# Kernel tuning notes

Hardware: AMD Instinct MI355X
Metric: run time of the kernel (lower is better)

The kernel has to match this reference:

```python
import jax, jax.numpy as jnp
import numpy as np

D = 1024
H = 16
FF = 4096
N, L = 16, 512
EPS = 1e-5


def _layernorm(x, g, b):
    mu = jnp.mean(x, axis=-1, keepdims=True)
    var = jnp.mean(jnp.square(x - mu), axis=-1, keepdims=True)
    return (x - mu) * jax.lax.rsqrt(var + EPS) * g + b


def setup_inputs() -> dict:
    key = jax.random.key(0)
    ks = jax.random.split(key, 8)
    std = 0.02  # truncated-normal-ish init scale
    return {
        "x": jax.random.normal(ks[0], (N, L, D), dtype=jnp.float32),
        "mask": jnp.zeros((N, L, L), dtype=bool),  # True = padded position
        "WQ": jax.random.normal(ks[1], (D, D), dtype=jnp.float32) * std,
        "bQ": jnp.zeros((D,), jnp.float32),
        "WK": jax.random.normal(ks[2], (D, D), dtype=jnp.float32) * std,
        "bK": jnp.zeros((D,), jnp.float32),
        "WV": jax.random.normal(ks[3], (D, D), dtype=jnp.float32) * std,
        "bV": jnp.zeros((D,), jnp.float32),
        "WO": jax.random.normal(ks[4], (D, D), dtype=jnp.float32) * std,
        "bO": jnp.zeros((D,), jnp.float32),
        "ln0_g": jnp.ones((D,), jnp.float32),
        "ln0_b": jnp.zeros((D,), jnp.float32),
        "W1": jax.random.normal(ks[5], (D, FF), dtype=jnp.float32) * std,
        "b1": jnp.zeros((FF,), jnp.float32),
        "W2": jax.random.normal(ks[6], (FF, D), dtype=jnp.float32) * std,
        "b2": jnp.zeros((D,), jnp.float32),
        "ln1_g": jnp.ones((D,), jnp.float32),
        "ln1_b": jnp.zeros((D,), jnp.float32),
    }


def reference(x, mask, WQ, bQ, WK, bK, WV, bV, WO, bO, ln0_g, ln0_b,
              W1, b1, W2, b2, ln1_g, ln1_b):
    n, l, d = x.shape
    dk = d // H
    scale = jnp.sqrt(jnp.float32(dk))
    # QKV projections -> [n, H, l, dk]
    q = (x @ WQ + bQ).reshape(n, l, H, dk).transpose(0, 2, 1, 3)
    k = (x @ WK + bK).reshape(n, l, H, dk).transpose(0, 2, 1, 3)
    v = (x @ WV + bV).reshape(n, l, H, dk).transpose(0, 2, 1, 3)
    scores = jnp.einsum('nhqd,nhkd->nhqk', q, k) / scale
    scores = jnp.where(mask[:, None, :, :], -jnp.inf, scores)
    attn = jax.nn.softmax(scores, axis=-1)
    attn = jnp.nan_to_num(attn, nan=0.0)  # fully-masked rows -> 0
    ctx = jnp.einsum('nhqk,nhkd->nhqd', attn, v).transpose(0, 2, 1, 3).reshape(n, l, d)
    mha = ctx @ WO + bO
    h = _layernorm(mha + x, ln0_g, ln0_b)
    ff = jax.nn.gelu(h @ W1 + b1, approximate=False) @ W2 + b2
    return _layernorm(ff + h, ln1_g, ln1_b)
```

## Files before the change

kernel.cpp:

```cpp
#include <hip/hip_runtime.h>
#include <math.h>

#define D_   1024
#define H_   16
#define DK_  64
#define L_   512
#define NB_  16
#define FF_  4096
#define M_   (NB_*L_)
#define EPS_ 1e-5f

typedef __attribute__((ext_vector_type(8))) __bf16 bf16x8;
typedef __attribute__((ext_vector_type(4))) float f32x4;
typedef __attribute__((ext_vector_type(4))) unsigned short us4;
typedef __attribute__((ext_vector_type(8))) unsigned short us8;
typedef __attribute__((ext_vector_type(4))) unsigned int u32x4;

__device__ __forceinline__ float gelu_exact(float x){
    return 0.5f * x * (1.f + erff(x * 0.7071067811865476f));
}

__device__ __forceinline__ unsigned split1(float a){
    unsigned ab = __builtin_bit_cast(unsigned, a);
    unsigned short h = (unsigned short)(ab >> 16);
    float hif = __builtin_bit_cast(float, ab & 0xffff0000u);
    float rem = a - hif;
    unsigned short lo = (unsigned short)(__builtin_bit_cast(unsigned, rem) >> 16);
    return (unsigned)h | ((unsigned)lo << 16);
}

__device__ __forceinline__ void split4v(float4 x, us4& h, us4& lo){
    unsigned p0 = split1(x.x), p1 = split1(x.y), p2 = split1(x.z), p3 = split1(x.w);
    h.x = (unsigned short)p0; lo.x = (unsigned short)(p0 >> 16);
    h.y = (unsigned short)p1; lo.y = (unsigned short)(p1 >> 16);
    h.z = (unsigned short)p2; lo.z = (unsigned short)(p2 >> 16);
    h.w = (unsigned short)p3; lo.w = (unsigned short)(p3 >> 16);
}

__device__ __forceinline__ void split8v(float4 x, float4 y, bf16x8& h, bf16x8& lo){
    us8 hu, lu; unsigned p;
    p = split1(x.x); hu[0]=(unsigned short)p; lu[0]=(unsigned short)(p>>16);
    p = split1(x.y); hu[1]=(unsigned short)p; lu[1]=(unsigned short)(p>>16);
    p = split1(x.z); hu[2]=(unsigned short)p; lu[2]=(unsigned short)(p>>16);
    p = split1(x.w); hu[3]=(unsigned short)p; lu[3]=(unsigned short)(p>>16);
    p = split1(y.x); hu[4]=(unsigned short)p; lu[4]=(unsigned short)(p>>16);
    p = split1(y.y); hu[5]=(unsigned short)p; lu[5]=(unsigned short)(p>>16);
    p = split1(y.z); hu[6]=(unsigned short)p; lu[6]=(unsigned short)(p>>16);
    p = split1(y.w); hu[7]=(unsigned short)p; lu[7]=(unsigned short)(p>>16);
    h = __builtin_bit_cast(bf16x8, hu);
    lo = __builtin_bit_cast(bf16x8, lu);
}

template<int EPI>
__global__ __launch_bounds__(256, 2)
void gemm_mfma(const float* __restrict__ A, const float* __restrict__ B,
               const float* __restrict__ bias, const float* __restrict__ res,
               float* __restrict__ C, int M, int N, int K)
{
    __shared__ __align__(16) unsigned short Ah[4096];
    __shared__ __align__(16) unsigned short Al[4096];
    __shared__ __align__(16) unsigned short Bh[4096];
    __shared__ __align__(16) unsigned short Bl[4096];

    const int t = threadIdx.x;
    const int bm = blockIdx.y * 128, bn = blockIdx.x * 128;
    const int l = t & 63, w = t >> 6, wr = w >> 1, wc = w & 1;

    size_t gA[4]; int lA[4];
#pragma unroll
    for (int i = 0; i < 4; ++i) {
        int f = t + 256 * i;
        int r = f >> 3, k0 = (f & 7) * 4;
        gA[i] = (size_t)(bm + r) * K + k0;
        lA[i] = ((r >> 4) << 9) + (((k0 >> 3) << 4) + (r & 15)) * 8 + (k0 & 7);
    }
    const int c = t & 127, kq = t >> 7;
    const size_t gB = (size_t)(kq * 16) * N + bn + c;
    const int lB = ((c >> 4) << 9) + (kq * 2 * 16 + (c & 15)) * 8;

    f32x4 acc[4][4] = {};

    float4 aA[4];
    float  bB[16];
#pragma unroll
    for (int i = 0; i < 4; ++i) aA[i] = *(const float4*)&A[gA[i]];
#pragma unroll
    for (int i = 0; i < 16; ++i) bB[i] = B[gB + (size_t)i * N];

    const int nk = K >> 5;
    for (int ks = 0; ks < nk; ++ks) {
        __syncthreads();
#pragma unroll
        for (int i = 0; i < 4; ++i) {
            us4 h, lo;
            split4v(aA[i], h, lo);
            *(us4*)&Ah[lA[i]] = h;
            *(us4*)&Al[lA[i]] = lo;
        }
        {
            us8 h0, l0, h1, l1;
#pragma unroll
            for (int i = 0; i < 8; ++i) {
                unsigned p = split1(bB[i]);
                h0[i] = (unsigned short)p; l0[i] = (unsigned short)(p >> 16);
            }
#pragma unroll
            for (int i = 0; i < 8; ++i) {
                unsigned p = split1(bB[8 + i]);
                h1[i] = (unsigned short)p; l1[i] = (unsigned short)(p >> 16);
            }
            *(us8*)&Bh[lB] = h0;       *(us8*)&Bl[lB] = l0;
            *(us8*)&Bh[lB + 128] = h1; *(us8*)&Bl[lB + 128] = l1;
        }
        __syncthreads();
        if (ks + 1 < nk) {
            const int ko = (ks + 1) * 32;
#pragma unroll
            for (int i = 0; i < 4; ++i) aA[i] = *(const float4*)&A[gA[i] + ko];
#pragma unroll
            for (int i = 0; i < 16; ++i) bB[i] = B[gB + (size_t)(ko + i) * N];
        }
        bf16x8 ah[4], al4[4];
#pragma unroll
        for (int m = 0; m < 4; ++m) {
            const int idx = (wr * 4 + m) * 512 + l * 8;
            ah[m]  = *(const bf16x8*)&Ah[idx];
            al4[m] = *(const bf16x8*)&Al[idx];
        }
#pragma unroll
        for (int n = 0; n < 4; ++n) {
            const int idx = (wc * 4 + n) * 512 + l * 8;
            bf16x8 bh = *(const bf16x8*)&Bh[idx];
            bf16x8 bl = *(const bf16x8*)&Bl[idx];
#pragma unroll
            for (int m = 0; m < 4; ++m) {
                acc[m][n] = __builtin_amdgcn_mfma_f32_16x16x32_bf16(ah[m],  bh, acc[m][n], 0, 0, 0);
                acc[m][n] = __builtin_amdgcn_mfma_f32_16x16x32_bf16(ah[m],  bl, acc[m][n], 0, 0, 0);
                acc[m][n] = __builtin_amdgcn_mfma_f32_16x16x32_bf16(al4[m], bh, acc[m][n], 0, 0, 0);
            }
        }
    }

#pragma unroll
    for (int n = 0; n < 4; ++n) {
        const int col = bn + wc * 64 + n * 16 + (l & 15);
        const float bv = bias[col];
#pragma unroll
        for (int m = 0; m < 4; ++m) {
            const int rowb = bm + wr * 64 + m * 16 + ((l >> 4) << 2);
#pragma unroll
            for (int j = 0; j < 4; ++j) {
                const int row = rowb + j;
                float v = acc[m][n][j] + bv;
                if (EPI == 0) {
                    const int nb = row >> 9, ll = row & (L_ - 1);
                    const int hh = col >> 6, d = col & (DK_ - 1);
                    C[(((size_t)nb * H_ + hh) * L_ + ll) * DK_ + d] = v;
                } else if (EPI == 1) {
                    v += res[(size_t)row * N + col];
                    C[(size_t)row * N + col] = v;
                } else if (EPI == 2) {
                    C[(size_t)row * N + col] = gelu_exact(v);
                } else {
                    const int nb = row >> 9, ll = row & (L_ - 1);
                    const int hh = col >> 6, d = col & (DK_ - 1);
                    C[(((size_t)nb * H_ + hh) * DK_ + d) * L_ + ll] = v;
                }
            }
        }
    }
}

__global__ __launch_bounds__(512, 1)
void attn_mfma(const float* __restrict__ qb, const float* __restrict__ kb,
               const float* __restrict__ vt, const unsigned char* __restrict__ mask,
               float* __restrict__ ctx)
{
    __shared__ unsigned Sp[64 * 512];
    __shared__ __align__(16) unsigned short KVh[4096];
    __shared__ __align__(16) unsigned short KVl[4096];

    const int t = threadIdx.x;
    const int l = t & 63, w = t >> 6;
    const int qsub = w & 3;
    const int ksub = w >> 2;
    const int qt = blockIdx.x;
    const int nh = blockIdx.y;
    const int n = nh >> 4, hh = nh & 15;
    const int q0 = qt * 64;

    const float* qbase = qb + (size_t)nh * L_ * DK_;
    const float* kbase = kb + (size_t)nh * L_ * DK_;
    const float* vbase = vt + (size_t)nh * DK_ * L_;

    bf16x8 qh[2], ql[2];
#pragma unroll
    for (int ks = 0; ks < 2; ++ks) {
        const size_t qa = (size_t)(q0 + qsub * 16 + (l & 15)) * DK_ + ks * 32 + (l >> 4) * 8;
        float4 a0 = *(const float4*)&qbase[qa];
        float4 a1 = *(const float4*)&qbase[qa + 4];
        split8v(a0, a1, qh[ks], ql[ks]);
    }

    float4 pf[2];
#pragma unroll
    for (int i = 0; i < 2; ++i) {
        int f = t + 512 * i, r = f >> 4, k0 = (f & 15) * 4;
        pf[i] = *(const float4*)&kbase[(size_t)r * DK_ + k0];
    }
    for (int kt = 0; kt < 8; ++kt) {
        __syncthreads();
#pragma unroll
        for (int i = 0; i < 2; ++i) {
            int f = t + 512 * i, r = f >> 4, k0 = (f & 15) * 4;
            int off = (((r >> 4) * 2 + (k0 >> 5)) << 9) + ((((k0 & 31) >> 3) << 4) + (r & 15)) * 8 + (k0 & 7);
            us4 h, lo; split4v(pf[i], h, lo);
            *(us4*)&KVh[off] = h; *(us4*)&KVl[off] = lo;
        }
        __syncthreads();
        if (kt < 7) {
#pragma unroll
            for (int i = 0; i < 2; ++i) {
                int f = t + 512 * i, r = f >> 4, k0 = (f & 15) * 4;
                pf[i] = *(const float4*)&kbase[(size_t)((kt + 1) * 64 + r) * DK_ + k0];
            }
        }
        f32x4 acc2[2] = {};
#pragma unroll
        for (int ks = 0; ks < 2; ++ks) {
#pragma unroll
            for (int b = 0; b < 2; ++b) {
                const int off = (((ksub * 2 + b) * 2 + ks) << 9) + l * 8;
                bf16x8 bh = *(const bf16x8*)&KVh[off];
                bf16x8 bl = *(const bf16x8*)&KVl[off];
                acc2[b] = __builtin_amdgcn_mfma_f32_16x16x32_bf16(qh[ks], bh, acc2[b], 0, 0, 0);
                acc2[b] = __builtin_amdgcn_mfma_f32_16x16x32_bf16(qh[ks], bl, acc2[b], 0, 0, 0);
                acc2[b] = __builtin_amdgcn_mfma_f32_16x16x32_bf16(ql[ks], bh, acc2[b], 0, 0, 0);
            }
        }
#pragma unroll
        for (int b = 0; b < 2; ++b) {
            const int col = kt * 64 + (ksub * 2 + b) * 16 + (l & 15);
#pragma unroll
            for (int j = 0; j < 4; ++j) {
                const int row = qsub * 16 + (l >> 4) * 4 + j;
                const int word = row * 512 + ((((col >> 2) ^ (row & 7)) << 2) | (col & 3));
                Sp[word] = split1(acc2[b][j] * 0.125f);
            }
        }
    }
    __syncthreads();

    {
        const int row = t >> 3, seg = t & 7;
        const unsigned* mrow = (const unsigned*)(mask + ((size_t)n * L_ + q0 + row) * L_ + seg * 64);
        unsigned mb[16];
#pragma unroll
        for (int j2 = 0; j2 < 16; ++j2) mb[j2] = mrow[j2];
        float sum = 0.f;
#pragma unroll
        for (int i = 0; i < 64; ++i) {
            const int col = seg * 64 + i;
            const int word = row * 512 + ((((col >> 2) ^ (row & 7)) << 2) | (i & 3));
            unsigned u = Sp[word];
            float val = __builtin_bit_cast(float, (u & 0xffffu) << 16)
                      + __builtin_bit_cast(float, u & 0xffff0000u);
            if (!((mb[i >> 2] >> ((i & 3) * 8)) & 0xffu)) sum += __expf(val);
        }
        sum += __shfl_xor(sum, 1); sum += __shfl_xor(sum, 2); sum += __shfl_xor(sum, 4);
        const float inv = sum > 0.f ? 1.f / sum : 0.f;
#pragma unroll
        for (int i = 0; i < 64; ++i) {
            const int col = seg * 64 + i;
            const int word = row * 512 + ((((col >> 2) ^ (row & 7)) << 2) | (i & 3));
            unsigned u = Sp[word];
            float val = __builtin_bit_cast(float, (u & 0xffffu) << 16)
                      + __builtin_bit_cast(float, u & 0xffff0000u);
            float p = ((mb[i >> 2] >> ((i & 3) * 8)) & 0xffu) ? 0.f : __expf(val) * inv;
            Sp[word] = split1(p);
        }
    }

    f32x4 oacc[2] = {};
#pragma unroll
    for (int i = 0; i < 2; ++i) {
        int f = t + 512 * i, d = f >> 4, key0 = (f & 15) * 4;
        pf[i] = *(const float4*)&vbase[(size_t)d * L_ + key0];
    }
    for (int kt = 0; kt < 8; ++kt) {
        __syncthreads();
#pragma unroll
        for (int i = 0; i < 2; ++i) {
            int f = t + 512 * i, d = f >> 4, key0 = (f & 15) * 4;
            int off = (((d >> 4) * 2 + (key0 >> 5)) << 9) + ((((key0 & 31) >> 3) << 4) + (d & 15)) * 8 + (key0 & 7);
            us4 h, lo; split4v(pf[i], h, lo);
            *(us4*)&KVh[off] = h; *(us4*)&KVl[off] = lo;
        }
        __syncthreads();
        if (kt < 7) {
#pragma unroll
            for (int i = 0; i < 2; ++i) {
                int f = t + 512 * i, d = f >> 4, key0 = (f & 15) * 4;
                pf[i] = *(const float4*)&vbase[(size_t)d * L_ + (kt + 1) * 64 + key0];
            }
        }
#pragma unroll
        for (int ks = 0; ks < 2; ++ks) {
            const int rowpv = qsub * 16 + (l & 15);
            const int sw = rowpv & 7;
            const int g0 = kt * 16 + ks * 8 + (l >> 4) * 2;
            u32x4 Ua = *(const u32x4*)&Sp[rowpv * 512 + ((g0 ^ sw) << 2)];
            u32x4 Ub = *(const u32x4*)&Sp[rowpv * 512 + (((g0 + 1) ^ sw) << 2)];
            us8 hu, lu;
            hu[0]=(unsigned short)Ua[0]; lu[0]=(unsigned short)(Ua[0]>>16);
            hu[1]=(unsigned short)Ua[1]; lu[1]=(unsigned short)(Ua[1]>>16);
            hu[2]=(unsigned short)Ua[2]; lu[2]=(unsigned short)(Ua[2]>>16);
            hu[3]=(unsigned short)Ua[3]; lu[3]=(unsigned short)(Ua[3]>>16);
            hu[4]=(unsigned short)Ub[0]; lu[4]=(unsigned short)(Ub[0]>>16);
            hu[5]=(unsigned short)Ub[1]; lu[5]=(unsigned short)(Ub[1]>>16);
            hu[6]=(unsigned short)Ub[2]; lu[6]=(unsigned short)(Ub[2]>>16);
            hu[7]=(unsigned short)Ub[3]; lu[7]=(unsigned short)(Ub[3]>>16);
            bf16x8 ph = __builtin_bit_cast(bf16x8, hu);
            bf16x8 pl = __builtin_bit_cast(bf16x8, lu);
#pragma unroll
            for (int b = 0; b < 2; ++b) {
                const int off = (((ksub * 2 + b) * 2 + ks) << 9) + l * 8;
                bf16x8 vh = *(const bf16x8*)&KVh[off];
                bf16x8 vl = *(const bf16x8*)&KVl[off];
                oacc[b] = __builtin_amdgcn_mfma_f32_16x16x32_bf16(ph, vh, oacc[b], 0, 0, 0);
                oacc[b] = __builtin_amdgcn_mfma_f32_16x16x32_bf16(ph, vl, oacc[b], 0, 0, 0);
                oacc[b] = __builtin_amdgcn_mfma_f32_16x16x32_bf16(pl, vh, oacc[b], 0, 0, 0);
            }
        }
    }
#pragma unroll
    for (int b = 0; b < 2; ++b) {
        const int col = ksub * 32 + b * 16 + (l & 15);
#pragma unroll
        for (int j = 0; j < 4; ++j) {
            const int rowl = q0 + qsub * 16 + (l >> 4) * 4 + j;
            ctx[((size_t)n * L_ + rowl) * D_ + hh * 64 + col] = oacc[b][j];
        }
    }
}

__global__ __launch_bounds__(256)
void ln_k(const float* __restrict__ in, const float* __restrict__ g,
          const float* __restrict__ b, float* __restrict__ out)
{
    const int row = blockIdx.x, tid = threadIdx.x;
    const float* p = in + (size_t)row * D_;
    float4 v = *(const float4*)&p[tid * 4];
    float s = v.x + v.y + v.z + v.w;
#pragma unroll
    for (int off = 32; off > 0; off >>= 1) s += __shfl_down(s, off);
    __shared__ float wsum[4];
    const int wid = tid >> 6, lane = tid & 63;
    if (lane == 0) wsum[wid] = s;
    __syncthreads();
    const float mu = (wsum[0] + wsum[1] + wsum[2] + wsum[3]) * (1.f / D_);
    const float dx = v.x - mu, dy = v.y - mu, dz = v.z - mu, dw = v.w - mu;
    float q = dx * dx + dy * dy + dz * dz + dw * dw;
#pragma unroll
    for (int off = 32; off > 0; off >>= 1) q += __shfl_down(q, off);
    __syncthreads();
    if (lane == 0) wsum[wid] = q;
    __syncthreads();
    const float var = (wsum[0] + wsum[1] + wsum[2] + wsum[3]) * (1.f / D_);
    const float rs = rsqrtf(var + EPS_);
    const float4 gg = *(const float4*)&g[tid * 4];
    const float4 bb = *(const float4*)&b[tid * 4];
    float4 o;
    o.x = dx * rs * gg.x + bb.x;
    o.y = dy * rs * gg.y + bb.y;
    o.z = dz * rs * gg.z + bb.z;
    o.w = dw * rs * gg.w + bb.w;
    *(float4*)&out[(size_t)row * D_ + tid * 4] = o;
}

extern "C" void kernel_launch(void* const* d_in, const int* in_sizes, int n_in,
                              void* d_out, int out_size, void* d_ws, size_t ws_size,
                              hipStream_t stream)
{
    const float* x  = (const float*)d_in[0];
    const unsigned char* mask = (const unsigned char*)d_in[1];
    const float* WQ = (const float*)d_in[2];
    const float* bQ = (const float*)d_in[3];
    const float* WK = (const float*)d_in[4];
    const float* bK = (const float*)d_in[5];
    const float* WV = (const float*)d_in[6];
    const float* bV = (const float*)d_in[7];
    const float* WO = (const float*)d_in[8];
    const float* bO = (const float*)d_in[9];
    const float* g0 = (const float*)d_in[10];
    const float* b0 = (const float*)d_in[11];
    const float* W1 = (const float*)d_in[12];
    const float* b1 = (const float*)d_in[13];
    const float* W2 = (const float*)d_in[14];
    const float* b2 = (const float*)d_in[15];
    const float* g1 = (const float*)d_in[16];
    const float* b1n = (const float*)d_in[17];
    float* out = (float*)d_out;

    const size_t MD = (size_t)M_ * D_;
    float* ws   = (float*)d_ws;
    float* qbuf = ws;
    float* kbuf = ws + MD;
    float* vbuf = ws + 2 * MD;
    float* cbuf = ws + 3 * MD;
    float* fbuf = ws + 4 * MD;
    float* hbuf = out;

    dim3 blk(256);
    dim3 gD(D_ / 128, M_ / 128);
    dim3 gF(FF_ / 128, M_ / 128);

    gemm_mfma<0><<<gD, blk, 0, stream>>>(x, WQ, bQ, nullptr, qbuf, M_, D_, D_);
    gemm_mfma<0><<<gD, blk, 0, stream>>>(x, WK, bK, nullptr, kbuf, M_, D_, D_);
    gemm_mfma<3><<<gD, blk, 0, stream>>>(x, WV, bV, nullptr, vbuf, M_, D_, D_);
    attn_mfma<<<dim3(L_ / 64, NB_ * H_), dim3(512), 0, stream>>>(qbuf, kbuf, vbuf, mask, cbuf);
    gemm_mfma<1><<<gD, blk, 0, stream>>>(cbuf, WO, bO, x, qbuf, M_, D_, D_);
    ln_k<<<dim3(M_), blk, 0, stream>>>(qbuf, g0, b0, hbuf);
    gemm_mfma<2><<<gF, blk, 0, stream>>>(hbuf, W1, b1, nullptr, fbuf, M_, FF_, D_);
    gemm_mfma<1><<<gD, blk, 0, stream>>>(fbuf, W2, b2, hbuf, kbuf, M_, D_, FF_);
    ln_k<<<dim3(M_), blk, 0, stream>>>(kbuf, g1, b1n, out);
}
```

Measured before the change: 1.109 ms.

## Pre-split weights into bf16 hi/lo tiles and stream them via global_load_lds

```diff
diff --git a/kernel.cpp b/kernel.cpp
--- a/kernel.cpp
+++ b/kernel.cpp
@@ -51,20 +51,51 @@
     lo = __builtin_bit_cast(bf16x8, lu);
 }
 
+__device__ __forceinline__ void gl16(const unsigned short* g, unsigned short* l){
+    __builtin_amdgcn_global_load_lds(
+        (const __attribute__((address_space(1))) unsigned int*)g,
+        (__attribute__((address_space(3))) unsigned int*)l, 16, 0, 0);
+}
+
+__global__ __launch_bounds__(256)
+void wsplit_k(const float* __restrict__ W, unsigned short* __restrict__ out,
+              int K, int N)
+{
+    const int ks = blockIdx.x, nb = blockIdx.y;
+    unsigned short* tb = out + ((size_t)nb * (K >> 5) + ks) * 8192;
+    const int t = threadIdx.x;
+#pragma unroll
+    for (int it = 0; it < 2; ++it) {
+        const int slot = t + it * 256;
+        const int c = slot & 127, ko = slot >> 7;
+        us8 h, lo;
+#pragma unroll
+        for (int j = 0; j < 8; ++j) {
+            float wv = W[(size_t)(ks * 32 + ko * 8 + j) * N + nb * 128 + c];
+            unsigned p = split1(wv);
+            h[j] = (unsigned short)p; lo[j] = (unsigned short)(p >> 16);
+        }
+        const int off = ((c >> 4) * 512) + (ko * 16 + (c & 15)) * 8;
+        *(us8*)&tb[off] = h;
+        *(us8*)&tb[4096 + off] = lo;
+    }
+}
+
 template<int EPI>
-__global__ __launch_bounds__(256, 2)
-void gemm_mfma(const float* __restrict__ A, const float* __restrict__ B,
+__global__ __launch_bounds__(256, 4)
+void gemm_mfma(const float* __restrict__ A, const unsigned short* __restrict__ Bw,
                const float* __restrict__ bias, const float* __restrict__ res,
                float* __restrict__ C, int M, int N, int K)
 {
-    __shared__ __align__(16) unsigned short Ah[4096];
-    __shared__ __align__(16) unsigned short Al[4096];
-    __shared__ __align__(16) unsigned short Bh[4096];
-    __shared__ __align__(16) unsigned short Bl[4096];
+    __shared__ __align__(16) unsigned short Ah[4160];
+    __shared__ __align__(16) unsigned short Al[4160];
+    __shared__ __align__(16) unsigned short Bs[8192];
 
     const int t = threadIdx.x;
-    const int bm = blockIdx.y * 128, bn = blockIdx.x * 128;
+    const int nb = blockIdx.x;
+    const int bm = blockIdx.y * 128, bn = nb * 128;
     const int l = t & 63, w = t >> 6, wr = w >> 1, wc = w & 1;
+    const int nk = K >> 5;
 
     size_t gA[4]; int lA[4];
 #pragma unroll
@@ -72,24 +103,23 @@
         int f = t + 256 * i;
         int r = f >> 3, k0 = (f & 7) * 4;
         gA[i] = (size_t)(bm + r) * K + k0;
-        lA[i] = ((r >> 4) << 9) + (((k0 >> 3) << 4) + (r & 15)) * 8 + (k0 & 7);
-    }
-    const int c = t & 127, kq = t >> 7;
-    const size_t gB = (size_t)(kq * 16) * N + bn + c;
-    const int lB = ((c >> 4) << 9) + (kq * 2 * 16 + (c & 15)) * 8;
+        lA[i] = (r >> 4) * 520 + (((k0 >> 3) << 4) + (r & 15)) * 8 + (k0 & 7);
+    }
+    const unsigned short* wtile = Bw + (size_t)nb * nk * 8192;
 
     f32x4 acc[4][4] = {};
 
     float4 aA[4];
-    float  bB[16];
 #pragma unroll
     for (int i = 0; i < 4; ++i) aA[i] = *(const float4*)&A[gA[i]];
-#pragma unroll
-    for (int i = 0; i < 16; ++i) bB[i] = B[gB + (size_t)i * N];
-
-    const int nk = K >> 5;
+
     for (int ks = 0; ks < nk; ++ks) {
         __syncthreads();
+        const unsigned short* tb = wtile + (size_t)ks * 8192;
+        gl16(tb + t * 8,        Bs + t * 8);
+        gl16(tb + 2048 + t * 8, Bs + 2048 + t * 8);
+        gl16(tb + 4096 + t * 8, Bs + 4096 + t * 8);
+        gl16(tb + 6144 + t * 8, Bs + 6144 + t * 8);
 #pragma unroll
         for (int i = 0; i < 4; ++i) {
             us4 h, lo;
@@ -97,41 +127,24 @@
             *(us4*)&Ah[lA[i]] = h;
             *(us4*)&Al[lA[i]] = lo;
         }
-        {
-            us8 h0, l0, h1, l1;
-#pragma unroll
-            for (int i = 0; i < 8; ++i) {
-                unsigned p = split1(bB[i]);
-                h0[i] = (unsigned short)p; l0[i] = (unsigned short)(p >> 16);
-            }
-#pragma unroll
-            for (int i = 0; i < 8; ++i) {
-                unsigned p = split1(bB[8 + i]);
-                h1[i] = (unsigned short)p; l1[i] = (unsigned short)(p >> 16);
-            }
-            *(us8*)&Bh[lB] = h0;       *(us8*)&Bl[lB] = l0;
-            *(us8*)&Bh[lB + 128] = h1; *(us8*)&Bl[lB + 128] = l1;
-        }
         __syncthreads();
         if (ks + 1 < nk) {
             const int ko = (ks + 1) * 32;
 #pragma unroll
             for (int i = 0; i < 4; ++i) aA[i] = *(const float4*)&A[gA[i] + ko];
-#pragma unroll
-            for (int i = 0; i < 16; ++i) bB[i] = B[gB + (size_t)(ko + i) * N];
         }
         bf16x8 ah[4], al4[4];
 #pragma unroll
         for (int m = 0; m < 4; ++m) {
-            const int idx = (wr * 4 + m) * 512 + l * 8;
+            const int idx = (wr * 4 + m) * 520 + l * 8;
             ah[m]  = *(const bf16x8*)&Ah[idx];
             al4[m] = *(const bf16x8*)&Al[idx];
         }
 #pragma unroll
         for (int n = 0; n < 4; ++n) {
             const int idx = (wc * 4 + n) * 512 + l * 8;
-            bf16x8 bh = *(const bf16x8*)&Bh[idx];
-            bf16x8 bl = *(const bf16x8*)&Bl[idx];
+            bf16x8 bh = *(const bf16x8*)&Bs[idx];
+            bf16x8 bl = *(const bf16x8*)&Bs[4096 + idx];
 #pragma unroll
             for (int m = 0; m < 4; ++m) {
                 acc[m][n] = __builtin_amdgcn_mfma_f32_16x16x32_bf16(ah[m],  bh, acc[m][n], 0, 0, 0);
@@ -153,18 +166,18 @@
                 const int row = rowb + j;
                 float v = acc[m][n][j] + bv;
                 if (EPI == 0) {
-                    const int nb = row >> 9, ll = row & (L_ - 1);
+                    const int nbx = row >> 9, ll = row & (L_ - 1);
                     const int hh = col >> 6, d = col & (DK_ - 1);
-                    C[(((size_t)nb * H_ + hh) * L_ + ll) * DK_ + d] = v;
+                    C[(((size_t)nbx * H_ + hh) * L_ + ll) * DK_ + d] = v;
                 } else if (EPI == 1) {
                     v += res[(size_t)row * N + col];
                     C[(size_t)row * N + col] = v;
                 } else if (EPI == 2) {
                     C[(size_t)row * N + col] = gelu_exact(v);
                 } else {
-                    const int nb = row >> 9, ll = row & (L_ - 1);
+                    const int nbx = row >> 9, ll = row & (L_ - 1);
                     const int hh = col >> 6, d = col & (DK_ - 1);
-                    C[(((size_t)nb * H_ + hh) * DK_ + d) * L_ + ll] = v;
+                    C[(((size_t)nbx * H_ + hh) * DK_ + d) * L_ + ll] = v;
                 }
             }
         }
@@ -411,17 +424,33 @@
     float* fbuf = ws + 4 * MD;
     float* hbuf = out;
 
+    unsigned short* WQs = (unsigned short*)fbuf;
+    unsigned short* WKs = WQs + 2ull * D_ * D_;
+    unsigned short* WVs = WQs + 4ull * D_ * D_;
+    unsigned short* WOs = WQs + 6ull * D_ * D_;
+    unsigned short* W1s = (unsigned short*)vbuf;
+    unsigned short* W2s = (unsigned short*)vbuf + 2ull * D_ * FF_;
+
     dim3 blk(256);
     dim3 gD(D_ / 128, M_ / 128);
     dim3 gF(FF_ / 128, M_ / 128);
 
-    gemm_mfma<0><<<gD, blk, 0, stream>>>(x, WQ, bQ, nullptr, qbuf, M_, D_, D_);
-    gemm_mfma<0><<<gD, blk, 0, stream>>>(x, WK, bK, nullptr, kbuf, M_, D_, D_);
-    gemm_mfma<3><<<gD, blk, 0, stream>>>(x, WV, bV, nullptr, vbuf, M_, D_, D_);
+    wsplit_k<<<dim3(D_ / 32, D_ / 128), blk, 0, stream>>>(WQ, WQs, D_, D_);
+    wsplit_k<<<dim3(D_ / 32, D_ / 128), blk, 0, stream>>>(WK, WKs, D_, D_);
+    wsplit_k<<<dim3(D_ / 32, D_ / 128), blk, 0, stream>>>(WV, WVs, D_, D_);
+    wsplit_k<<<dim3(D_ / 32, D_ / 128), blk, 0, stream>>>(WO, WOs, D_, D_);
+
+    gemm_mfma<0><<<gD, blk, 0, stream>>>(x, WQs, bQ, nullptr, qbuf, M_, D_, D_);
+    gemm_mfma<0><<<gD, blk, 0, stream>>>(x, WKs, bK, nullptr, kbuf, M_, D_, D_);
+    gemm_mfma<3><<<gD, blk, 0, stream>>>(x, WVs, bV, nullptr, vbuf, M_, D_, D_);
     attn_mfma<<<dim3(L_ / 64, NB_ * H_), dim3(512), 0, stream>>>(qbuf, kbuf, vbuf, mask, cbuf);
-    gemm_mfma<1><<<gD, blk, 0, stream>>>(cbuf, WO, bO, x, qbuf, M_, D_, D_);
+    gemm_mfma<1><<<gD, blk, 0, stream>>>(cbuf, WOs, bO, x, qbuf, M_, D_, D_);
     ln_k<<<dim3(M_), blk, 0, stream>>>(qbuf, g0, b0, hbuf);
-    gemm_mfma<2><<<gF, blk, 0, stream>>>(hbuf, W1, b1, nullptr, fbuf, M_, FF_, D_);
-    gemm_mfma<1><<<gD, blk, 0, stream>>>(fbuf, W2, b2, hbuf, kbuf, M_, D_, FF_);
+
+    wsplit_k<<<dim3(D_ / 32, FF_ / 128), blk, 0, stream>>>(W1, W1s, D_, FF_);
+    wsplit_k<<<dim3(FF_ / 32, D_ / 128), blk, 0, stream>>>(W2, W2s, FF_, D_);
+
+    gemm_mfma<2><<<gF, blk, 0, stream>>>(hbuf, W1s, b1, nullptr, fbuf, M_, FF_, D_);
+    gemm_mfma<1><<<gD, blk, 0, stream>>>(fbuf, W2s, b2, hbuf, kbuf, M_, D_, FF_);
     ln_k<<<dim3(M_), blk, 0, stream>>>(kbuf, g1, b1n, out);
 }
```

Result: slower. 1.745 ms (+57.4%).
